# Kernel optimization log

Measured on AMD Instinct MI355X. Metric: run time of the kernel, lower is better.

Reference implementation:

```python
import jax, jax.numpy as jnp
import numpy as np

NH = 4          # num_heads
EPS = 1e-6
GATE_CAP = 15.0
LOGIT_CAP = 30.0


def soft_cap(x, cap):
    return cap * jnp.tanh(x / cap)


def rms_norm(x, w, eps=EPS):
    xf = x.astype(jnp.float32)
    scale = jax.lax.rsqrt(jnp.mean(xf * xf, axis=-1, keepdims=True) + eps)
    return (xf * scale).astype(x.dtype) * w


def multihead_layernorm(h, w, eps=EPS):
    # h: [B, NH, S, DH]; LayerNorm over DH per head, weight over NH*DH
    hf = h.astype(jnp.float32)
    mu = jnp.mean(hf, axis=-1, keepdims=True)
    var = jnp.mean((hf - mu) ** 2, axis=-1, keepdims=True)
    hn = ((hf - mu) * jax.lax.rsqrt(var + eps)).astype(h.dtype)
    B, nh, S, DH = h.shape
    hn = hn.transpose(0, 2, 1, 3).reshape(B, S, nh * DH)  # [B,S,v_dim]
    return hn * w


def mlstm_parallel(q, k, v, i_pre, f_pre, eps=EPS):
    # q,k: [B,NH,S,Dqk]; v: [B,NH,S,Dv]; i_pre,f_pre: [B,NH,S]
    S = q.shape[2]
    dqk = q.shape[-1]
    logf = jax.nn.log_sigmoid(f_pre.astype(jnp.float32))      # [B,NH,S]
    F = jnp.cumsum(logf, axis=-1)
    # logD[t,s] = F[t] - F[s] + i[s]  for s <= t
    logD = F[..., :, None] - F[..., None, :] + i_pre.astype(jnp.float32)[..., None, :]
    mask = jnp.tril(jnp.ones((S, S), dtype=bool))
    logD = jnp.where(mask, logD, -jnp.inf)
    m = jnp.max(logD, axis=-1, keepdims=True)                  # [B,NH,S,1]
    Dmat = jnp.exp(logD - m)
    scores = jnp.einsum('bhsd,bhtd->bhst', q, k) / jnp.sqrt(float(dqk))
    C = scores * Dmat                                          # [B,NH,S,S]
    n = jnp.maximum(jnp.abs(C.sum(-1)), jnp.exp(-m[..., 0]))   # [B,NH,S]
    h = jnp.einsum('bhst,bhtd->bhsd', C, v) / (n[..., None] + eps)
    return h


def block(x, p):
    (n1, wq, wk, wv, wog, wi, bi, wf, bf, mhw, wout, n2, wg, wu, wd) = p
    B, S, D = x.shape
    xm = rms_norm(x, n1)
    q = xm @ wq.T
    k = xm @ wk.T
    v = xm @ wv.T
    o_pre = xm @ wog.T
    i_pre = soft_cap(xm @ wi.T + bi, GATE_CAP)   # [B,S,NH]
    f_pre = soft_cap(xm @ wf.T + bf, GATE_CAP)
    q = q.reshape(B, S, NH, -1).transpose(0, 2, 1, 3)
    k = k.reshape(B, S, NH, -1).transpose(0, 2, 1, 3)
    v = v.reshape(B, S, NH, -1).transpose(0, 2, 1, 3)
    h = mlstm_parallel(q, k, v, i_pre.transpose(0, 2, 1), f_pre.transpose(0, 2, 1))
    hn = multihead_layernorm(h, mhw)             # [B,S,v_dim]
    y = (hn * jax.nn.sigmoid(o_pre)) @ wout.T
    x = x + y
    xf = rms_norm(x, n2)
    ff = (jax.nn.silu(xf @ wg.T) * (xf @ wu.T)) @ wd.T
    return x + ff


def setup_inputs() -> dict:
    key = jax.random.key(0)
    ks = jax.random.split(key, 16)
    L, D, V, UP, QK = 2, 1024, 32000, 2752, 512
    s = 0.02
    return {
        'tokens': jax.random.randint(ks[0], (1, 2048), 0, V),
        'emb': jax.random.normal(ks[1], (V, D)) * s,
        'norm1_w': jnp.ones((L, D)),
        'Wq': jax.random.normal(ks[2], (L, QK, D)) * s,
        'Wk': jax.random.normal(ks[3], (L, QK, D)) * s,
        'Wv': jax.random.normal(ks[4], (L, D, D)) * s,
        'Wog': jax.random.normal(ks[5], (L, D, D)) * s,
        'Wi': jax.random.normal(ks[6], (L, NH, D)) * s,
        'bi': jax.random.normal(ks[7], (L, NH)) * s,
        'Wf': jax.random.normal(ks[8], (L, NH, D)) * s,
        'bf': jnp.ones((L, NH)) * 3.0,
        'mh_w': jnp.ones((L, D)),
        'Wout': jax.random.normal(ks[9], (L, D, D)) * s,
        'norm2_w': jnp.ones((L, D)),
        'Wg': jax.random.normal(ks[10], (L, UP, D)) * s,
        'Wu': jax.random.normal(ks[11], (L, UP, D)) * s,
        'Wd': jax.random.normal(ks[12], (L, D, UP)) * s,
        'out_norm_w': jnp.ones((D,)),
        'Wlm': jax.random.normal(ks[13], (V, D)) * s,
    }


def reference(tokens, emb, norm1_w, Wq, Wk, Wv, Wog, Wi, bi, Wf, bf, mh_w,
              Wout, norm2_w, Wg, Wu, Wd, out_norm_w, Wlm):
    x = emb[tokens]                    # [B,S,D]
    L = Wq.shape[0]
    for l in range(L):
        p = (norm1_w[l], Wq[l], Wk[l], Wv[l], Wog[l], Wi[l], bi[l], Wf[l],
             bf[l], mh_w[l], Wout[l], norm2_w[l], Wg[l], Wu[l], Wd[l])
        x = block(x, p)
    x = rms_norm(x, out_norm_w)
    logits = x @ Wlm.T
    return soft_cap(logits, LOGIT_CAP)
```

## Files before the change

### kernel.cpp

```cpp
#include <hip/hip_runtime.h>
#include <hip/hip_bf16.h>
#include <math.h>


#define S_LEN 2048
#define DMODEL 1024
#define WLAYER 12845056

typedef __attribute__((ext_vector_type(8))) __bf16 bf16x8;
typedef __attribute__((ext_vector_type(8))) unsigned short u16x8;
typedef __attribute__((ext_vector_type(4))) unsigned short u16x4;
typedef __attribute__((ext_vector_type(4))) float f32x4v;

union cvu { u16x8 u; bf16x8 b; };

__device__ __forceinline__ unsigned short bf_us(float f) {
  union { __bf16 b; unsigned short u; } c;
  c.b = (__bf16)f;
  return c.u;
}
__device__ __forceinline__ float us_f(unsigned short u) {
  union { __bf16 b; unsigned short u; } c;
  c.u = u;
  return (float)c.b;
}
__device__ __forceinline__ bf16x8 ld_bf8(const unsigned short* p, int byte_off) {
  cvu c;
  c.u = *(const u16x8*)((const char*)p + byte_off);
  return c.b;
}
__device__ __forceinline__ float fast_sigmoid(float v) {
  return 1.0f / (1.0f + __expf(-v));
}
__device__ __forceinline__ float fast_softcap30(float v) {
  float e = __expf(-fabsf(v) * (1.0f / 15.0f));
  float t = (1.0f - e) / (1.0f + e);
  return copysignf(30.0f * t, v);
}

#define AS_G __attribute__((address_space(1)))
#define AS_L __attribute__((address_space(3)))

__device__ __forceinline__ void stage64(const unsigned short* gbase, int K,
                                        unsigned short* lds, int wave, int lane, int k0) {
#pragma unroll
  for (int j = 0; j < 4; ++j) {
    const int rbase = (j * 4 + wave) * 8;
    const int r = rbase + (lane >> 3);
    const int cg = (lane & 7) ^ (r & 7);
    const unsigned short* src = gbase + (size_t)r * K + k0 + cg * 8;
    __builtin_amdgcn_global_load_lds((const AS_G void*)src,
                                     (AS_L void*)(lds + rbase * 64), 16, 0, 0);
  }
}

__global__ __launch_bounds__(256) void embed_kernel(
    const int* __restrict__ tok, const float* __restrict__ emb, float* __restrict__ x) {
  int s = blockIdx.x;
  int t = tok[s];
  const float4 v = *(const float4*)(emb + (size_t)t * DMODEL + threadIdx.x * 4);
  *(float4*)(x + (size_t)s * DMODEL + threadIdx.x * 4) = v;
}

__global__ __launch_bounds__(256) void rmsnorm_kernel(
    const float* __restrict__ x, const float* __restrict__ w,
    unsigned short* __restrict__ outb) {
  int s = blockIdx.x, tid = threadIdx.x;
  const float* xr = x + (size_t)s * DMODEL;
  float4 v = *(const float4*)(xr + tid * 4);
  float ss = v.x * v.x + v.y * v.y + v.z * v.z + v.w * v.w;
#pragma unroll
  for (int off = 32; off > 0; off >>= 1) ss += __shfl_down(ss, off);
  __shared__ float red[4];
  if ((tid & 63) == 0) red[tid >> 6] = ss;
  __syncthreads();
  float tot = red[0] + red[1] + red[2] + red[3];
  float scale = rsqrtf(tot * (1.0f / DMODEL) + 1e-6f);
  float4 wv = *(const float4*)(w + tid * 4);
  u16x4 ub;
  ub[0] = bf_us(v.x * scale * wv.x);
  ub[1] = bf_us(v.y * scale * wv.y);
  ub[2] = bf_us(v.z * scale * wv.z);
  ub[3] = bf_us(v.w * scale * wv.w);
  *(u16x4*)(outb + (size_t)s * DMODEL + tid * 4) = ub;
}

__global__ __launch_bounds__(256) void wcvt8_kernel(
    const float* __restrict__ Wq, const float* __restrict__ Wk,
    const float* __restrict__ Wv, const float* __restrict__ Wog,
    const float* __restrict__ Wout, const float* __restrict__ Wg,
    const float* __restrict__ Wu, const float* __restrict__ Wd,
    const float* __restrict__ Wlm,
    unsigned short* __restrict__ W, unsigned short* __restrict__ Wlm16) {
  const size_t de = ((size_t)blockIdx.x * 256 + threadIdx.x) * 8;
  if (de >= 2ull * WLAYER) {
    size_t i = de - 2ull * WLAYER;
    float4 a0 = *(const float4*)(Wlm + i);
    float4 a1 = *(const float4*)(Wlm + i + 4);
    u16x8 o;
    o[0] = bf_us(a0.x); o[1] = bf_us(a0.y); o[2] = bf_us(a0.z); o[3] = bf_us(a0.w);
    o[4] = bf_us(a1.x); o[5] = bf_us(a1.y); o[6] = bf_us(a1.z); o[7] = bf_us(a1.w);
    *(u16x8*)(Wlm16 + i) = o;
    return;
  }
  int e = (int)de, l = 0;
  if (e >= WLAYER) { l = 1; e -= WLAYER; }
  const float* src = nullptr;
  size_t idx = 0;
  if (e < 524288)       { src = Wq  + (size_t)l * 524288;  idx = e; }
  else if (e < 1048576) { src = Wk  + (size_t)l * 524288;  idx = e - 524288; }
  else if (e < 2097152) { src = Wv  + (size_t)l * 1048576; idx = e - 1048576; }
  else if (e < 3145728) { src = Wog + (size_t)l * 1048576; idx = e - 2097152; }
  else if (e < 4194304) { src = Wout + (size_t)l * 1048576; idx = e - 3145728; }
  else if (e < 7077888) {
    int t = e - 4194304, row = t >> 10;
    if (row < 2752) { src = Wg + (size_t)l * 2818048; idx = t; }
  } else if (e < 9961472) {
    int t = e - 7077888, row = t >> 10;
    if (row < 2752) { src = Wu + (size_t)l * 2818048; idx = t; }
  } else {
    int t = e - 9961472, row = t / 2816, col = t - row * 2816;
    if (col < 2752) { src = Wd + (size_t)l * 2818048; idx = row * 2752 + col; }
  }
  u16x8 o;
  if (src) {
    float4 a0 = *(const float4*)(src + idx);
    float4 a1 = *(const float4*)(src + idx + 4);
    o[0] = bf_us(a0.x); o[1] = bf_us(a0.y); o[2] = bf_us(a0.z); o[3] = bf_us(a0.w);
    o[4] = bf_us(a1.x); o[5] = bf_us(a1.y); o[6] = bf_us(a1.z); o[7] = bf_us(a1.w);
  } else {
#pragma unroll
    for (int k = 0; k < 8; ++k) o[k] = 0;
  }
  *(u16x8*)(W + de) = o;
}

template <int EPI>
__global__ __launch_bounds__(256) void gemm_bb_kernel(
    const unsigned short* __restrict__ A, const unsigned short* __restrict__ B,
    const void* Xv, void* Cv, int K, int ldc) {
  __shared__ __align__(16) unsigned short As[128 * 64];
  __shared__ __align__(16) unsigned short Bs[128 * 64];
  const int tid = threadIdx.x;
  const int wave = tid >> 6, lane = tid & 63;
  const int gx = gridDim.x;
  const int nwg = gx * gridDim.y;
  const int d = blockIdx.y * gx + blockIdx.x;
  const int q = nwg >> 3;
  const int lgc = (d & 7) * q + (d >> 3);
  const int bm = (lgc % gx) * 128, bn = (lgc / gx) * 128;
  const int wr = (wave >> 1) * 64, wc = (wave & 1) * 64;
  const int lr = lane & 15, lhi = lane >> 4;
  const unsigned short* Ab = A + (size_t)bm * K;
  const unsigned short* Bb = B + (size_t)bn * K;
  f32x4v acc[4][4] = {};

  const int NK = K >> 6;
  for (int it = 0; it < NK; ++it) {
    stage64(Ab, K, As, wave, lane, it << 6);
    stage64(Bb, K, Bs, wave, lane, it << 6);
    __syncthreads();
#pragma unroll
    for (int kk = 0; kk < 2; ++kk) {
      const int sw = (((kk * 4 + lhi) ^ (lr & 7)) << 3);
      bf16x8 af[4], bfr[4];
#pragma unroll
      for (int mi = 0; mi < 4; ++mi) af[mi] = *(const bf16x8*)&As[(wr + mi * 16 + lr) * 64 + sw];
#pragma unroll
      for (int ni = 0; ni < 4; ++ni) bfr[ni] = *(const bf16x8*)&Bs[(wc + ni * 16 + lr) * 64 + sw];
#pragma unroll
      for (int mi = 0; mi < 4; ++mi)
#pragma unroll
        for (int ni = 0; ni < 4; ++ni)
          acc[mi][ni] = __builtin_amdgcn_mfma_f32_16x16x32_bf16(af[mi], bfr[ni], acc[mi][ni], 0, 0, 0);
    }
    __syncthreads();
  }
#pragma unroll
  for (int mi = 0; mi < 4; ++mi) {
#pragma unroll
    for (int ni = 0; ni < 4; ++ni) {
#pragma unroll
      for (int j = 0; j < 4; ++j) {
        int row = bm + wr + mi * 16 + lhi * 4 + j;
        int col = bn + wc + ni * 16 + lr;
        float v = acc[mi][ni][j];
        if (EPI == 0)
          ((float*)Cv)[(size_t)row * ldc + col] = v;
        if (EPI == 1)
          ((float*)Cv)[(size_t)row * ldc + col] = v + ((const float*)Xv)[(size_t)row * ldc + col];
      }
    }
  }
}

__global__ __launch_bounds__(512, 2) void lm256_kernel(
    const unsigned short* __restrict__ A, const unsigned short* __restrict__ B,
    float* __restrict__ C) {
  __shared__ __align__(16) unsigned short SH[3 * 16384];
  const int K = 1024, N = 32000, NT = 32;
  const int tid = threadIdx.x;
  const int wave = tid >> 6, lane = tid & 63;
  const int lr = lane & 15, lg = lane >> 4;
  const int wm = wave >> 2, wn = wave & 3;
  const int d = blockIdx.y * 8 + blockIdx.x;
  const int lgc = (d & 7) * 125 + (d >> 3);
  const int bm = (lgc & 7) * 256;
  const int bn = (lgc >> 3) * 256;
  const unsigned short* Ab = A + (size_t)bm * K;
  const unsigned short* Bb = B + (size_t)bn * K;

  auto stageM = [&](const unsigned short* gbase, unsigned short* lds, int k0) {
#pragma unroll
    for (int j = 0; j < 2; ++j) {
      const int r = j * 128 + wave * 16 + (lane >> 2);
      const int cg = (lane & 3) ^ ((r >> 1) & 3);
      const unsigned short* src = gbase + (size_t)r * K + k0 + cg * 8;
      __builtin_amdgcn_global_load_lds((const AS_G void*)src,
                                       (AS_L void*)(lds + (j * 128 + wave * 16) * 32), 16, 0, 0);
    }
  };
  auto stageT = [&](int tau) {
    unsigned short* base = SH + (tau % 3) * 16384;
    stageM(Ab, base, tau * 32);
    stageM(Bb, base + 8192, tau * 32);
  };

  f32x4v acc[8][4] = {};
  stageT(0);
  stageT(1);
  for (int t = 0; t < NT; ++t) {
    if (t < NT - 1) asm volatile("s_waitcnt vmcnt(4)" ::: "memory");
    else            asm volatile("s_waitcnt vmcnt(0)" ::: "memory");
    asm volatile("s_barrier" ::: "memory");
    if (t + 2 < NT) stageT(t + 2);
    const unsigned short* Al = SH + (t % 3) * 16384;
    const unsigned short* Bl = Al + 8192;
    bf16x8 bfr[4];
#pragma unroll
    for (int ni = 0; ni < 4; ++ni) {
      int row = wn * 64 + ni * 16 + lr;
      bfr[ni] = *(const bf16x8*)&Bl[row * 32 + ((lg ^ ((row >> 1) & 3)) << 3)];
    }
#pragma unroll
    for (int mi = 0; mi < 8; ++mi) {
      int row = wm * 128 + mi * 16 + lr;
      bf16x8 af = *(const bf16x8*)&Al[row * 32 + ((lg ^ ((row >> 1) & 3)) << 3)];
      __builtin_amdgcn_s_setprio(1);
#pragma unroll
      for (int ni = 0; ni < 4; ++ni)
        acc[mi][ni] = __builtin_amdgcn_mfma_f32_16x16x32_bf16(af, bfr[ni], acc[mi][ni], 0, 0, 0);
      __builtin_amdgcn_s_setprio(0);
    }
  }
#pragma unroll
  for (int mi = 0; mi < 8; ++mi)
#pragma unroll
    for (int ni = 0; ni < 4; ++ni)
#pragma unroll
      for (int jj = 0; jj < 4; ++jj) {
        int row = bm + wm * 128 + mi * 16 + lg * 4 + jj;
        int col = bn + wn * 64 + ni * 16 + lr;
        C[(size_t)row * N + col] = fast_softcap30(acc[mi][ni][jj]);
      }
}

__global__ __launch_bounds__(256) void qkvo_kernel(
    const unsigned short* __restrict__ A, const unsigned short* __restrict__ Wq16,
    const unsigned short* __restrict__ Wk16, const unsigned short* __restrict__ Wv16,
    const unsigned short* __restrict__ Wog16,
    unsigned short* __restrict__ qb, unsigned short* __restrict__ kb,
    unsigned short* __restrict__ vTb, float* __restrict__ og) {
  __shared__ __align__(16) unsigned short SH[2 * 128 * 64];
  unsigned short* Asb = SH;
  unsigned short* Bsb = SH + 128 * 64;
  const int tid = threadIdx.x;
  const int wave = tid >> 6, lane = tid & 63;
  const int gx = gridDim.x;
  const int nwg = gx * gridDim.y;
  const int dd = blockIdx.y * gx + blockIdx.x;
  const int qq = nwg >> 3;
  const int lgc = (dd & 7) * qq + (dd >> 3);
  const int bm = (lgc % gx) * 128;
  const int by = lgc / gx;
  const unsigned short* B;
  int bnl, mode;
  if (by < 4)       { B = Wq16;  bnl = by * 128;        mode = 0; }
  else if (by < 8)  { B = Wk16;  bnl = (by - 4) * 128;  mode = 1; }
  else if (by < 16) { B = Wv16;  bnl = (by - 8) * 128;  mode = 2; }
  else              { B = Wog16; bnl = (by - 16) * 128; mode = 3; }
  const int K = 1024;
  const int wr = (wave >> 1) * 64, wc = (wave & 1) * 64;
  const int lr = lane & 15, lhi = lane >> 4;
  const unsigned short* Ab = A + (size_t)bm * K;
  const unsigned short* Bb = B + (size_t)bnl * K;
  f32x4v acc[4][4] = {};

  for (int it = 0; it < 16; ++it) {
    stage64(Ab, K, Asb, wave, lane, it << 6);
    stage64(Bb, K, Bsb, wave, lane, it << 6);
    __syncthreads();
#pragma unroll
    for (int kk = 0; kk < 2; ++kk) {
      const int sw = (((kk * 4 + lhi) ^ (lr & 7)) << 3);
      bf16x8 af[4], bfr[4];
#pragma unroll
      for (int mi = 0; mi < 4; ++mi) af[mi] = *(const bf16x8*)&Asb[(wr + mi * 16 + lr) * 64 + sw];
#pragma unroll
      for (int ni = 0; ni < 4; ++ni) bfr[ni] = *(const bf16x8*)&Bsb[(wc + ni * 16 + lr) * 64 + sw];
#pragma unroll
      for (int mi = 0; mi < 4; ++mi)
#pragma unroll
        for (int ni = 0; ni < 4; ++ni)
          acc[mi][ni] = __builtin_amdgcn_mfma_f32_16x16x32_bf16(af[mi], bfr[ni], acc[mi][ni], 0, 0, 0);
    }
    __syncthreads();
  }
  if (mode == 2) {
#pragma unroll
    for (int mi = 0; mi < 4; ++mi)
#pragma unroll
      for (int ni = 0; ni < 4; ++ni)
#pragma unroll
        for (int j = 0; j < 4; ++j) {
          int row = wr + mi * 16 + lhi * 4 + j;
          int col = wc + ni * 16 + lr;
          int byte = col * 256 + ((((row >> 3) ^ (col & 7)) << 4)) + (row & 7) * 2;
          *(unsigned short*)((char*)SH + byte) = bf_us(acc[mi][ni][j]);
        }
    __syncthreads();
#pragma unroll
    for (int i = 0; i < 8; ++i) {
      int c = i * 16 + (tid >> 4);
      int rg = tid & 15;
      u16x8 u = *(const u16x8*)((const char*)SH + c * 256 + ((rg ^ (c & 7)) << 4));
      *(u16x8*)(vTb + (size_t)(bnl + c) * S_LEN + bm + rg * 8) = u;
    }
  } else {
#pragma unroll
    for (int mi = 0; mi < 4; ++mi)
#pragma unroll
      for (int ni = 0; ni < 4; ++ni)
#pragma unroll
        for (int j = 0; j < 4; ++j) {
          int row = bm + wr + mi * 16 + lhi * 4 + j;
          int col = bnl + wc + ni * 16 + lr;
          if (mode == 0)      qb[(size_t)row * 512 + col] = bf_us(acc[mi][ni][j]);
          else if (mode == 1) kb[(size_t)row * 512 + col] = bf_us(acc[mi][ni][j]);
          else                og[(size_t)row * 1024 + col] = acc[mi][ni][j];
        }
  }
}

__global__ __launch_bounds__(256) void ffn_kernel(
    const unsigned short* __restrict__ A, const unsigned short* __restrict__ Bg,
    const unsigned short* __restrict__ Bu, unsigned short* __restrict__ Gb) {
  __shared__ __align__(16) unsigned short As[128 * 64];
  __shared__ __align__(16) unsigned short Bgs[128 * 64];
  __shared__ __align__(16) unsigned short Bus[128 * 64];
  const int K = 1024;
  const int tid = threadIdx.x;
  const int wave = tid >> 6, lane = tid & 63;
  const int gx = gridDim.x;
  const int nwg = gx * gridDim.y;
  const int dd = blockIdx.y * gx + blockIdx.x;
  const int qq = nwg >> 3;
  const int lgc = (dd & 7) * qq + (dd >> 3);
  const int bm = (lgc % gx) * 128;
  const int bn = (lgc / gx) * 128;
  const int wr = (wave >> 1) * 64, wc = (wave & 1) * 64;
  const int lr = lane & 15, lhi = lane >> 4;
  const unsigned short* Ab = A + (size_t)bm * K;
  const unsigned short* Bgb = Bg + (size_t)bn * K;
  const unsigned short* Bub = Bu + (size_t)bn * K;
  f32x4v accg[4][4] = {};
  f32x4v accu[4][4] = {};
  for (int it = 0; it < 16; ++it) {
    stage64(Ab, K, As, wave, lane, it << 6);
    stage64(Bgb, K, Bgs, wave, lane, it << 6);
    stage64(Bub, K, Bus, wave, lane, it << 6);
    __syncthreads();
#pragma unroll
    for (int kk = 0; kk < 2; ++kk) {
      const int sw = (((kk * 4 + lhi) ^ (lr & 7)) << 3);
      bf16x8 af[4], bg[4], bu[4];
#pragma unroll
      for (int mi = 0; mi < 4; ++mi) af[mi] = *(const bf16x8*)&As[(wr + mi * 16 + lr) * 64 + sw];
#pragma unroll
      for (int ni = 0; ni < 4; ++ni) bg[ni] = *(const bf16x8*)&Bgs[(wc + ni * 16 + lr) * 64 + sw];
#pragma unroll
      for (int ni = 0; ni < 4; ++ni) bu[ni] = *(const bf16x8*)&Bus[(wc + ni * 16 + lr) * 64 + sw];
#pragma unroll
      for (int mi = 0; mi < 4; ++mi)
#pragma unroll
        for (int ni = 0; ni < 4; ++ni) {
          accg[mi][ni] = __builtin_amdgcn_mfma_f32_16x16x32_bf16(af[mi], bg[ni], accg[mi][ni], 0, 0, 0);
          accu[mi][ni] = __builtin_amdgcn_mfma_f32_16x16x32_bf16(af[mi], bu[ni], accu[mi][ni], 0, 0, 0);
        }
    }
    __syncthreads();
  }
#pragma unroll
  for (int mi = 0; mi < 4; ++mi) {
#pragma unroll
    for (int ni = 0; ni < 4; ++ni) {
#pragma unroll
      for (int j = 0; j < 4; ++j) {
        int row = bm + wr + mi * 16 + lhi * 4 + j;
        int col = bn + wc + ni * 16 + lr;
        float g = accg[mi][ni][j];
        float sv = g * fast_sigmoid(g) * accu[mi][ni][j];
        Gb[(size_t)row * 2816 + col] = bf_us(sv);
      }
    }
  }
}

__global__ __launch_bounds__(256) void gates_kernel(
    const float* __restrict__ x, const float* __restrict__ n1,
    const float* __restrict__ Wi, const float* __restrict__ bi,
    const float* __restrict__ Wf, const float* __restrict__ bfv,
    float* __restrict__ ipre, float* __restrict__ fpre) {
  int s = blockIdx.x;
  int head = threadIdx.x >> 6, lane = threadIdx.x & 63;
  const float* xr = x + (size_t)s * DMODEL;
  float xv[16];
  float ss = 0.f;
#pragma unroll
  for (int j = 0; j < 16; ++j) { xv[j] = xr[lane + j * 64]; ss += xv[j] * xv[j]; }
#pragma unroll
  for (int off = 32; off > 0; off >>= 1) ss += __shfl_xor(ss, off);
  float scale = rsqrtf(ss * (1.0f / DMODEL) + 1e-6f);
  const float* wi = Wi + head * DMODEL;
  const float* wf = Wf + head * DMODEL;
  float si = 0.f, sf = 0.f;
#pragma unroll
  for (int j = 0; j < 16; ++j) {
    int c = lane + j * 64;
    float xm = xv[j] * scale * n1[c];
    si += xm * wi[c];
    sf += xm * wf[c];
  }
#pragma unroll
  for (int off = 32; off > 0; off >>= 1) {
    si += __shfl_down(si, off);
    sf += __shfl_down(sf, off);
  }
  if (lane == 0) {
    ipre[head * S_LEN + s] = 15.0f * tanhf((si + bi[head]) * (1.0f / 15.0f));
    fpre[head * S_LEN + s] = 15.0f * tanhf((sf + bfv[head]) * (1.0f / 15.0f));
  }
}

__global__ __launch_bounds__(256) void scan_kernel(
    const float* __restrict__ ipre, const float* __restrict__ fpre,
    float* __restrict__ garr, float* __restrict__ Marr, float* __restrict__ earr) {
  const int h = threadIdx.x >> 6;
  const int lane = threadIdx.x & 63;
  const int base = h * S_LEN + lane * 32;
  float lf[32];
  float lsum = 0.f;
#pragma unroll
  for (int e = 0; e < 32; ++e) {
    float f = fpre[base + e];
    float v = fminf(f, 0.f) - log1pf(expf(-fabsf(f)));
    lf[e] = v;
    lsum += v;
  }
  float scan = lsum;
#pragma unroll
  for (int off = 1; off < 64; off <<= 1) {
    float t = __shfl_up(scan, off);
    if (lane >= off) scan += t;
  }
  float F0 = scan - lsum;
  float gv[32];
  float F = F0, lmax = -1e30f;
#pragma unroll
  for (int e = 0; e < 32; ++e) {
    F += lf[e];
    float g = ipre[base + e] - F;
    gv[e] = g;
    lmax = fmaxf(lmax, g);
    garr[base + e] = g;
  }
  float ms = lmax;
#pragma unroll
  for (int off = 1; off < 64; off <<= 1) {
    float t = __shfl_up(ms, off);
    if (lane >= off) ms = fmaxf(ms, t);
  }
  float em = __shfl_up(ms, 1);
  if (lane == 0) em = -1e30f;
  float run = em;
  F = F0;
#pragma unroll
  for (int e = 0; e < 32; ++e) {
    F += lf[e];
    run = fmaxf(run, gv[e]);
    Marr[base + e] = run;
    earr[base + e] = expf(-(F + run));
  }
}

__global__ __launch_bounds__(256) void mlstm_mfma_kernel(
    const unsigned short* __restrict__ Q, const unsigned short* __restrict__ Kb,
    const unsigned short* __restrict__ vT, const float* __restrict__ garr,
    const float* __restrict__ Marr,
    float* __restrict__ hp, float* __restrict__ npart) {
  const int h = blockIdx.y;
  const int T = blockIdx.x;
  const int sp = blockIdx.z;
  float* hpart = hp + (size_t)sp * 2097152;
  const int tid = threadIdx.x;
  const int w = tid >> 6, l = tid & 63;
  const int lr = l & 15, lg = l >> 4;
  const int hbase = h * S_LEN;
  const int sr = tid >> 4;
  const int sc = tid & 15;

  __shared__ __align__(16) unsigned short Ks[64 * 128];
  __shared__ __align__(16) unsigned short Vs[256 * 64];
  __shared__ __align__(16) unsigned short Ps[64 * 64];

  bf16x8 qf[4];
  {
    const unsigned short* qrow = Q + (size_t)(T * 64 + w * 16 + lr) * 512 + h * 128 + lg * 8;
#pragma unroll
    for (int kt = 0; kt < 4; ++kt) {
      cvu c;
      c.u = *(const u16x8*)(qrow + kt * 32);
      qf[kt] = c.b;
    }
  }
  float Mt[4];
#pragma unroll
  for (int j = 0; j < 4; ++j) Mt[j] = Marr[hbase + T * 64 + w * 16 + lg * 4 + j];

  f32x4v pv[16] = {};
  float nacc[4] = {0.f, 0.f, 0.f, 0.f};
  const float rs = 0.08838834764831845f;

  for (int ch = sp; ch <= T; ch += 4) {
    const int s0 = ch * 64;
    __syncthreads();
#pragma unroll
    for (int i = 0; i < 4; ++i) {
      int r = i * 16 + sr;
      u16x8 u = *(const u16x8*)(Kb + (size_t)(s0 + r) * 512 + h * 128 + sc * 8);
      int byte = r * 256 + ((sc * 16) ^ ((r & 7) << 4));
      *(u16x8*)((char*)Ks + byte) = u;
    }
#pragma unroll
    for (int i = 0; i < 16; ++i) {
      int r = i * 16 + sr;
      u16x4 u = *(const u16x4*)(vT + (size_t)(h * 256 + r) * S_LEN + s0 + sc * 4);
      int byte = r * 128 + ((sc * 8) ^ ((r & 7) << 4));
      *(u16x4*)((char*)Vs + byte) = u;
    }
    __syncthreads();
    f32x4v sa[4] = {};
#pragma unroll
    for (int ni = 0; ni < 4; ++ni) {
#pragma unroll
      for (int kt = 0; kt < 4; ++kt) {
        int row = ni * 16 + lr;
        int byte = row * 256 + (((kt * 32 + lg * 8) * 2) ^ ((row & 7) << 4));
        bf16x8 kf = ld_bf8(Ks, byte);
        sa[ni] = __builtin_amdgcn_mfma_f32_16x16x32_bf16(qf[kt], kf, sa[ni], 0, 0, 0);
      }
    }
#pragma unroll
    for (int ni = 0; ni < 4; ++ni) {
      int sl = ni * 16 + lr;
      int sg = s0 + sl;
      float gv = garr[hbase + sg];
#pragma unroll
      for (int j = 0; j < 4; ++j) {
        int tloc = w * 16 + lg * 4 + j;
        int tg = T * 64 + tloc;
        float wgt = (sg <= tg) ? __expf(gv - Mt[j]) : 0.f;
        float val = sa[ni][j] * rs * wgt;
        nacc[j] += val;
        int byte = tloc * 128 + ((sl * 2) ^ ((tloc & 7) << 4));
        *(unsigned short*)((char*)Ps + byte) = bf_us(val);
      }
    }
#pragma unroll
    for (int kt2 = 0; kt2 < 2; ++kt2) {
      int tloc = w * 16 + lr;
      int sb = (kt2 * 32 + lg * 8) * 2;
      bf16x8 pa = ld_bf8(Ps, tloc * 128 + (sb ^ ((tloc & 7) << 4)));
#pragma unroll
      for (int nv = 0; nv < 16; ++nv) {
        int dv = nv * 16 + lr;
        bf16x8 vb = ld_bf8(Vs, dv * 128 + (sb ^ ((dv & 7) << 4)));
        pv[nv] = __builtin_amdgcn_mfma_f32_16x16x32_bf16(pa, vb, pv[nv], 0, 0, 0);
      }
    }
  }
#pragma unroll
  for (int j = 0; j < 4; ++j) {
#pragma unroll
    for (int off = 1; off < 16; off <<= 1) nacc[j] += __shfl_xor(nacc[j], off);
  }
#pragma unroll
  for (int j = 0; j < 4; ++j) {
    int tg = T * 64 + w * 16 + lg * 4 + j;
    if (lr == 0) npart[sp * 8192 + hbase + tg] = nacc[j];
    float* orow = hpart + (size_t)tg * DMODEL + h * 256;
#pragma unroll
    for (int nvt = 0; nvt < 16; ++nvt) orow[nvt * 16 + lr] = pv[nvt][j];
  }
}

__global__ __launch_bounds__(256) void mhln_gate_kernel(
    const float* __restrict__ hp, const float* __restrict__ npart,
    const float* __restrict__ earr, const float* __restrict__ mhw,
    const float* __restrict__ og, unsigned short* __restrict__ gact) {
  int s = blockIdx.x;
  int head = threadIdx.x >> 6, lane = threadIdx.x & 63;
  float n = (npart[head * S_LEN + s] + npart[8192 + head * S_LEN + s]) +
            (npart[16384 + head * S_LEN + s] + npart[24576 + head * S_LEN + s]);
  float nvv = fmaxf(fabsf(n), earr[head * S_LEN + s]);
  float inv = 1.0f / (nvv + 1e-6f);
  const size_t base = (size_t)s * DMODEL + head * 256;
  float vq[4];
#pragma unroll
  for (int qy = 0; qy < 4; ++qy) {
    size_t o = base + qy * 64 + lane;
    vq[qy] = ((hp[o] + hp[o + 2097152]) + (hp[o + 4194304] + hp[o + 6291456])) * inv;
  }
  float sum = vq[0] + vq[1] + vq[2] + vq[3];
#pragma unroll
  for (int off = 32; off > 0; off >>= 1) sum += __shfl_xor(sum, off);
  float mu = sum * (1.0f / 256.0f);
  float d0 = vq[0] - mu, d1 = vq[1] - mu, d2 = vq[2] - mu, d3 = vq[3] - mu;
  float vs = d0 * d0 + d1 * d1 + d2 * d2 + d3 * d3;
#pragma unroll
  for (int off = 32; off > 0; off >>= 1) vs += __shfl_xor(vs, off);
  float rstd = rsqrtf(vs * (1.0f / 256.0f) + 1e-6f);
  float dn[4] = {d0, d1, d2, d3};
#pragma unroll
  for (int qy = 0; qy < 4; ++qy) {
    int c = head * 256 + qy * 64 + lane;
    float ov = og[(size_t)s * DMODEL + c];
    gact[(size_t)s * DMODEL + c] = bf_us(dn[qy] * rstd * mhw[c] * fast_sigmoid(ov));
  }
}

extern "C" void kernel_launch(void* const* d_in, const int* in_sizes, int n_in,
                              void* d_out, int out_size, void* d_ws, size_t ws_size,
                              hipStream_t stream) {
  (void)in_sizes; (void)n_in; (void)out_size; (void)ws_size;
  const int*   tok   = (const int*)d_in[0];
  const float* emb   = (const float*)d_in[1];
  const float* norm1 = (const float*)d_in[2];
  const float* Wq    = (const float*)d_in[3];
  const float* Wk    = (const float*)d_in[4];
  const float* Wv    = (const float*)d_in[5];
  const float* Wog   = (const float*)d_in[6];
  const float* Wi    = (const float*)d_in[7];
  const float* bi    = (const float*)d_in[8];
  const float* Wf    = (const float*)d_in[9];
  const float* bfp   = (const float*)d_in[10];
  const float* mhw   = (const float*)d_in[11];
  const float* Wout  = (const float*)d_in[12];
  const float* norm2 = (const float*)d_in[13];
  const float* Wg    = (const float*)d_in[14];
  const float* Wu    = (const float*)d_in[15];
  const float* Wd    = (const float*)d_in[16];
  const float* onw   = (const float*)d_in[17];
  const float* Wlm   = (const float*)d_in[18];

  char* wsb = (char*)d_ws;
  const size_t MB = 1ull << 20;
  float*          x    = (float*)wsb;
  unsigned short* xmb  = (unsigned short*)(wsb + 8 * MB);
  float*          ipre = (float*)(wsb + 12 * MB);
  float*          fpre = ipre + 8192;
  float*          garr = fpre + 8192;
  float*          Marr = garr + 8192;
  float*          earr = Marr + 8192;
  float*          npart = earr + 8192;
  unsigned short* W16  = (unsigned short*)(wsb + 13 * MB);
  const size_t OQ = 0, OKk = 524288, OV = 1048576, OOG = 2097152, OOUT = 3145728,
               OGt = 4194304, OU = 7077888, OD = 9961472;
  unsigned short* qb    = (unsigned short*)(wsb + 62 * MB);
  unsigned short* kb    = (unsigned short*)(wsb + 64 * MB);
  unsigned short* vTb   = (unsigned short*)(wsb + 66 * MB);
  float*          og    = (float*)(wsb + 70 * MB);
  float*          hp    = (float*)(wsb + 78 * MB);
  unsigned short* gact  = (unsigned short*)(wsb + 110 * MB);
  unsigned short* Gb16  = (unsigned short*)(wsb + 114 * MB);
  unsigned short* wlm16 = (unsigned short*)(wsb + 126 * MB);

  embed_kernel<<<2048, 256, 0, stream>>>(tok, emb, x);
  wcvt8_kernel<<<28544, 256, 0, stream>>>(Wq, Wk, Wv, Wog, Wout, Wg, Wu, Wd, Wlm,
                                          W16, wlm16);

  for (int l = 0; l < 2; ++l) {
    const unsigned short* Wl = W16 + (size_t)l * WLAYER;
    const float* n1   = norm1 + (size_t)l * 1024;
    const float* wiv  = Wi   + (size_t)l * 4 * 1024;
    const float* bil  = bi   + (size_t)l * 4;
    const float* wfv  = Wf   + (size_t)l * 4 * 1024;
    const float* bfl  = bfp  + (size_t)l * 4;
    const float* mhwl = mhw  + (size_t)l * 1024;
    const float* n2   = norm2 + (size_t)l * 1024;

    rmsnorm_kernel<<<2048, 256, 0, stream>>>(x, n1, xmb);
    qkvo_kernel<<<dim3(16, 24), 256, 0, stream>>>(xmb, Wl + OQ, Wl + OKk, Wl + OV,
                                                  Wl + OOG, qb, kb, vTb, og);
    gates_kernel<<<2048, 256, 0, stream>>>(x, n1, wiv, bil, wfv, bfl, ipre, fpre);
    scan_kernel<<<1, 256, 0, stream>>>(ipre, fpre, garr, Marr, earr);
    mlstm_mfma_kernel<<<dim3(32, 4, 4), 256, 0, stream>>>(qb, kb, vTb, garr, Marr,
                                                          hp, npart);
    mhln_gate_kernel<<<2048, 256, 0, stream>>>(hp, npart, earr, mhwl, og, gact);
    gemm_bb_kernel<1><<<dim3(16, 8), 256, 0, stream>>>(gact, Wl + OOUT, x, x, 1024, 1024);
    rmsnorm_kernel<<<2048, 256, 0, stream>>>(x, n2, xmb);
    ffn_kernel<<<dim3(16, 22), 256, 0, stream>>>(xmb, Wl + OGt, Wl + OU, Gb16);
    gemm_bb_kernel<1><<<dim3(16, 8), 256, 0, stream>>>(Gb16, Wl + OD, x, x, 2816, 1024);
  }

  rmsnorm_kernel<<<2048, 256, 0, stream>>>(x, onw, xmb);
  lm256_kernel<<<dim3(8, 125), 512, 0, stream>>>(xmb, wlm16, (float*)d_out);
}
```

Before: 810.1 us.

## Triple-buffer GEMM K-loop with 32-wide async LDS staging and prefetch depth two

The bf16 GEMM kernels (generic and QKVO projection) change from a single-buffered 64-wide K step with two barriers per iteration to a three-slot ring of 32-wide K tiles. Two tiles are loaded ahead via global_load_lds, and each iteration uses one barrier plus a vmcnt wait. This is meant to hide global-load latency behind MFMA work and cut barrier stalls, and s_setprio raises wave priority around the MFMA block. In exchange it uses more LDS (48KB), which may reduce occupancy, and it does twice as many loop iterations with half the MFMAs per barrier.

```diff
diff --git a/kernel.cpp b/kernel.cpp
--- a/kernel.cpp
+++ b/kernel.cpp
@@ -51,6 +51,18 @@
     const unsigned short* src = gbase + (size_t)r * K + k0 + cg * 8;
     __builtin_amdgcn_global_load_lds((const AS_G void*)src,
                                      (AS_L void*)(lds + rbase * 64), 16, 0, 0);
+  }
+}
+
+__device__ __forceinline__ void stage32(const unsigned short* gbase, int K,
+                                        unsigned short* lds, int wave, int lane, int k0) {
+#pragma unroll
+  for (int j = 0; j < 2; ++j) {
+    const int r = j * 64 + wave * 16 + (lane >> 2);
+    const int cg = (lane & 3) ^ ((r >> 1) & 3);
+    const unsigned short* src = gbase + (size_t)r * K + k0 + cg * 8;
+    __builtin_amdgcn_global_load_lds((const AS_G void*)src,
+                                     (AS_L void*)(lds + (j * 64 + wave * 16) * 32), 16, 0, 0);
   }
 }
 
@@ -139,8 +151,7 @@
 __global__ __launch_bounds__(256) void gemm_bb_kernel(
     const unsigned short* __restrict__ A, const unsigned short* __restrict__ B,
     const void* Xv, void* Cv, int K, int ldc) {
-  __shared__ __align__(16) unsigned short As[128 * 64];
-  __shared__ __align__(16) unsigned short Bs[128 * 64];
+  __shared__ __align__(16) unsigned short SH[3 * 8192];
   const int tid = threadIdx.x;
   const int wave = tid >> 6, lane = tid & 63;
   const int gx = gridDim.x;
@@ -155,26 +166,40 @@
   const unsigned short* Bb = B + (size_t)bn * K;
   f32x4v acc[4][4] = {};
 
-  const int NK = K >> 6;
-  for (int it = 0; it < NK; ++it) {
-    stage64(Ab, K, As, wave, lane, it << 6);
-    stage64(Bb, K, Bs, wave, lane, it << 6);
-    __syncthreads();
-#pragma unroll
-    for (int kk = 0; kk < 2; ++kk) {
-      const int sw = (((kk * 4 + lhi) ^ (lr & 7)) << 3);
-      bf16x8 af[4], bfr[4];
-#pragma unroll
-      for (int mi = 0; mi < 4; ++mi) af[mi] = *(const bf16x8*)&As[(wr + mi * 16 + lr) * 64 + sw];
-#pragma unroll
-      for (int ni = 0; ni < 4; ++ni) bfr[ni] = *(const bf16x8*)&Bs[(wc + ni * 16 + lr) * 64 + sw];
-#pragma unroll
-      for (int mi = 0; mi < 4; ++mi)
-#pragma unroll
-        for (int ni = 0; ni < 4; ++ni)
-          acc[mi][ni] = __builtin_amdgcn_mfma_f32_16x16x32_bf16(af[mi], bfr[ni], acc[mi][ni], 0, 0, 0);
-    }
-    __syncthreads();
+  auto stageT = [&](int tau) {
+    unsigned short* base = SH + (tau % 3) * 8192;
+    stage32(Ab, K, base, wave, lane, tau * 32);
+    stage32(Bb, K, base + 4096, wave, lane, tau * 32);
+  };
+
+  const int NT = K >> 5;
+  stageT(0);
+  stageT(1);
+  for (int t = 0; t < NT; ++t) {
+    if (t < NT - 1) asm volatile("s_waitcnt vmcnt(4)" ::: "memory");
+    else            asm volatile("s_waitcnt vmcnt(0)" ::: "memory");
+    asm volatile("s_barrier" ::: "memory");
+    if (t + 2 < NT) stageT(t + 2);
+    const unsigned short* Al = SH + (t % 3) * 8192;
+    const unsigned short* Bl = Al + 4096;
+    bf16x8 af[4], bfr[4];
+#pragma unroll
+    for (int mi = 0; mi < 4; ++mi) {
+      int row = wr + mi * 16 + lr;
+      af[mi] = *(const bf16x8*)&Al[row * 32 + ((lhi ^ ((row >> 1) & 3)) << 3)];
+    }
+#pragma unroll
+    for (int ni = 0; ni < 4; ++ni) {
+      int row = wc + ni * 16 + lr;
+      bfr[ni] = *(const bf16x8*)&Bl[row * 32 + ((lhi ^ ((row >> 1) & 3)) << 3)];
+    }
+    __builtin_amdgcn_s_setprio(1);
+#pragma unroll
+    for (int mi = 0; mi < 4; ++mi)
+#pragma unroll
+      for (int ni = 0; ni < 4; ++ni)
+        acc[mi][ni] = __builtin_amdgcn_mfma_f32_16x16x32_bf16(af[mi], bfr[ni], acc[mi][ni], 0, 0, 0);
+    __builtin_amdgcn_s_setprio(0);
   }
 #pragma unroll
   for (int mi = 0; mi < 4; ++mi) {
@@ -271,9 +296,7 @@
     const unsigned short* __restrict__ Wog16,
     unsigned short* __restrict__ qb, unsigned short* __restrict__ kb,
     unsigned short* __restrict__ vTb, float* __restrict__ og) {
-  __shared__ __align__(16) unsigned short SH[2 * 128 * 64];
-  unsigned short* Asb = SH;
-  unsigned short* Bsb = SH + 128 * 64;
+  __shared__ __align__(16) unsigned short SH[3 * 8192];
   const int tid = threadIdx.x;
   const int wave = tid >> 6, lane = tid & 63;
   const int gx = gridDim.x;
@@ -296,27 +319,43 @@
   const unsigned short* Bb = B + (size_t)bnl * K;
   f32x4v acc[4][4] = {};
 
-  for (int it = 0; it < 16; ++it) {
-    stage64(Ab, K, Asb, wave, lane, it << 6);
-    stage64(Bb, K, Bsb, wave, lane, it << 6);
+  auto stageT = [&](int tau) {
+    unsigned short* base = SH + (tau % 3) * 8192;
+    stage32(Ab, K, base, wave, lane, tau * 32);
+    stage32(Bb, K, base + 4096, wave, lane, tau * 32);
+  };
+
+  const int NT = 32;
+  stageT(0);
+  stageT(1);
+  for (int t = 0; t < NT; ++t) {
+    if (t < NT - 1) asm volatile("s_waitcnt vmcnt(4)" ::: "memory");
+    else            asm volatile("s_waitcnt vmcnt(0)" ::: "memory");
+    asm volatile("s_barrier" ::: "memory");
+    if (t + 2 < NT) stageT(t + 2);
+    const unsigned short* Al = SH + (t % 3) * 8192;
+    const unsigned short* Bl = Al + 4096;
+    bf16x8 af[4], bfr[4];
+#pragma unroll
+    for (int mi = 0; mi < 4; ++mi) {
+      int row = wr + mi * 16 + lr;
+      af[mi] = *(const bf16x8*)&Al[row * 32 + ((lhi ^ ((row >> 1) & 3)) << 3)];
+    }
+#pragma unroll
+    for (int ni = 0; ni < 4; ++ni) {
+      int row = wc + ni * 16 + lr;
+      bfr[ni] = *(const bf16x8*)&Bl[row * 32 + ((lhi ^ ((row >> 1) & 3)) << 3)];
+    }
+    __builtin_amdgcn_s_setprio(1);
+#pragma unroll
+    for (int mi = 0; mi < 4; ++mi)
+#pragma unroll
+      for (int ni = 0; ni < 4; ++ni)
+        acc[mi][ni] = __builtin_amdgcn_mfma_f32_16x16x32_bf16(af[mi], bfr[ni], acc[mi][ni], 0, 0, 0);
+    __builtin_amdgcn_s_setprio(0);
+  }
+  if (mode == 2) {
     __syncthreads();
-#pragma unroll
-    for (int kk = 0; kk < 2; ++kk) {
-      const int sw = (((kk * 4 + lhi) ^ (lr & 7)) << 3);
-      bf16x8 af[4], bfr[4];
-#pragma unroll
-      for (int mi = 0; mi < 4; ++mi) af[mi] = *(const bf16x8*)&Asb[(wr + mi * 16 + lr) * 64 + sw];
-#pragma unroll
-      for (int ni = 0; ni < 4; ++ni) bfr[ni] = *(const bf16x8*)&Bsb[(wc + ni * 16 + lr) * 64 + sw];
-#pragma unroll
-      for (int mi = 0; mi < 4; ++mi)
-#pragma unroll
-        for (int ni = 0; ni < 4; ++ni)
-          acc[mi][ni] = __builtin_amdgcn_mfma_f32_16x16x32_bf16(af[mi], bfr[ni], acc[mi][ni], 0, 0, 0);
-    }
-    __syncthreads();
-  }
-  if (mode == 2) {
 #pragma unroll
     for (int mi = 0; mi < 4; ++mi)
 #pragma unroll
```

Result: faster. 731.3 us (-9.7%).
